# Kernel optimization log

Measured on AMD Instinct MI355X. Metric: run time of the kernel, lower is better.

## Reference

```python
import jax, jax.numpy as jnp
import numpy as np

F = 3          # features
E = 2 * F      # transformer d_model
H = F          # n_heads (head_dim = 2)
FF = 2048      # torch TransformerEncoderLayer default dim_feedforward
OUT = 4
STRIDE = 2
N_BATCH = 16
T_LEN = 2046
LN_EPS = 1e-5


def setup_inputs() -> dict:
    key = jax.random.key(0)
    ks = iter(jax.random.split(key, 48))

    def p(shape, s=0.1):
        return jax.random.normal(next(ks), shape, dtype=jnp.float32) * s

    inp = {
        "x": jax.random.normal(next(ks), (N_BATCH, T_LEN, F), dtype=jnp.float32),
        # multi-scale depthwise conv kernels/biases
        "k64": p((8, F, 64)), "b64": p((8, F)),
        "k16": p((F, 16)), "b16": p((F,)),
        "k8": p((F, 8)), "b8": p((F,)),
        # stage-2 width-3 channel convs
        "kw3": p((F, 3)), "bw3": p((F,)),
        "km3": p((F, 3)), "bm3": p((F,)),
        "kn3": p((F, 3)), "bn3": p((F,)),
        # hidden FCs
        "fc1_w": p((6 * F, 12 * F)), "fc1_b": p((6 * F,)),
        "fc2_w": p((E, 6 * F)), "fc2_b": p((E,)),
        # 2 transformer encoder layers (stacked along leading dim)
        "inw": p((2, 3 * E, E)), "inb": p((2, 3 * E)),
        "ow": p((2, E, E)), "ob": p((2, E)),
        "l1w": jnp.ones((2, E), jnp.float32), "l1b": jnp.zeros((2, E), jnp.float32),
        "l2w": jnp.ones((2, E), jnp.float32), "l2b": jnp.zeros((2, E), jnp.float32),
        "f1w": p((2, FF, E)), "f1b": p((2, FF)),
        "f2w": p((2, E, FF)), "f2b": p((2, E)),
        # output head
        "out1_w": p((7, E)), "out1_b": p((7,)),
        "out2_w": p((OUT, 7)),
    }
    return inp


def _ln(y, w, b):
    mu = y.mean(-1, keepdims=True)
    var = ((y - mu) ** 2).mean(-1, keepdims=True)
    return (y - mu) / jnp.sqrt(var + LN_EPS) * w + b


def _conv3_same(y, k, b):
    # depthwise width-3 'same' conv over seq dim; y:(N,L,F), k:(F,3), b:(F,)
    yp = jnp.pad(y, ((0, 0), (1, 1), (0, 0)))
    return k[:, 0] * yp[:, :-2] + k[:, 1] * yp[:, 1:-1] + k[:, 2] * yp[:, 2:] + b


def _forward(x, k64, b64, k16, b16, k8, b8, kw3, bw3, km3, bm3, kn3, bn3,
             fc1_w, fc1_b, fc2_w, fc2_b, inw, inb, ow, ob,
             l1w, l1b, l2w, l2b, f1w, f1b, f2w, f2b, out1_w, out1_b, out2_w):
    N, T, _ = x.shape
    PAD = 40
    px = jnp.pad(x, ((0, 0), (PAD, PAD), (0, 0)))
    W = T // STRIDE + 1
    centers = PAD + 1 + STRIDE * jnp.arange(W)  # wide window centers
    starts = centers - 32
    relu = jax.nn.relu

    # wide: 8 depthwise width-64 kernels per center -> (N, 8W, F)
    wwin = px[:, centers[:, None] + jnp.arange(-32, 32), :]        # (N,W,64,F)
    wide = jnp.einsum('nwtf,kft->nwkf', wwin, k64) + b64[None, None]
    wide = wide.reshape(N, 8 * W, F)  # center-major, kernel-minor (loop order)

    # mid: width-16 kernel at 8 centers per window -> (N, 8W, F)
    mid_c = (starts[:, None] + 8 * jnp.arange(8)).reshape(-1)
    mwin = px[:, mid_c[:, None] + jnp.arange(-8, 8), :]            # (N,8W,16,F)
    mid = jnp.einsum('nctf,ft->ncf', mwin, k16) + b16

    # narrow: width-8 kernel at 32 centers per window, then maxpool4 -> (N, 8W, F)
    nar_c = (starts[:, None] + 2 * jnp.arange(32)).reshape(-1)
    nwin = px[:, nar_c[:, None] + jnp.arange(-4, 4), :]            # (N,32W,8,F)
    nar = jnp.einsum('nctf,ft->ncf', nwin, k8) + b8
    nar = nar.reshape(N, 8 * W, 4, F).max(axis=2)

    wide = 5.0 * relu(wide)  # residual=0, dropout=0 -> drop is identity
    mid = relu(mid)
    nar = relu(nar)

    wide = relu(_conv3_same(wide, kw3, bw3))
    mid = relu(_conv3_same(mid, km3, bm3))
    nar = relu(_conv3_same(nar, kn3, bn3))

    def pool2(y):  # MaxPool1d(2) over seq dim
        return y.reshape(N, 4 * W, 2, F).max(axis=2)
    wide, mid, nar = pool2(wide), pool2(mid), pool2(nar)

    S = W  # (4W) // 4 blocks

    def blocks(y):  # (N,4W,F) -> (N,S,4F), time-major flatten per block
        return y.reshape(N, S, 4 * F)
    flat = jnp.concatenate([blocks(wide), blocks(mid), blocks(nar)], axis=-1)

    h = relu(flat @ fc1_w.T + fc1_b)  # residual=0 -> (1-residual)*h + 0
    h = relu(h @ fc2_w.T + fc2_b)     # (N,S,E)
    seq = jnp.transpose(h, (1, 0, 2))  # (S,N,E), torch seq-first layout

    d = E // H
    scale = 1.0 / jnp.sqrt(jnp.float32(d))
    for l in range(2):  # post-LN TransformerEncoder, 2 layers
        qkv = seq @ inw[l].T + inb[l]                 # (S,N,3E)
        q, k_, v = jnp.split(qkv, 3, axis=-1)
        q = q.reshape(S, N, H, d)
        k_ = k_.reshape(S, N, H, d)
        v = v.reshape(S, N, H, d)
        att = jnp.einsum('snhd,tnhd->nhst', q, k_) * scale
        p_att = jax.nn.softmax(att, axis=-1)
        o = jnp.einsum('nhst,tnhd->snhd', p_att, v).reshape(S, N, E)
        o = o @ ow[l].T + ob[l]
        seq = _ln(seq + o, l1w[l], l1b[l])
        ff = relu(seq @ f1w[l].T + f1b[l]) @ f2w[l].T + f2b[l]
        seq = _ln(seq + ff, l2w[l], l2b[l])

    pooled = relu(seq.mean(axis=0))           # AvgPool1d over full seq -> (N,E)
    o1 = relu(pooled @ out1_w.T + out1_b)
    logits = o1 @ out2_w.T                    # no bias
    return jax.nn.log_softmax(logits, axis=1)


def reference(x, k64, b64, k16, b16, k8, b8, kw3, bw3, km3, bm3, kn3, bn3,
              fc1_w, fc1_b, fc2_w, fc2_b, inw, inb, ow, ob,
              l1w, l1b, l2w, l2b, f1w, f1b, f2w, f2b, out1_w, out1_b, out2_w):
    return _forward(x, k64, b64, k16, b16, k8, b8, kw3, bw3, km3, bm3, kn3, bn3,
                    fc1_w, fc1_b, fc2_w, fc2_b, inw, inb, ow, ob,
                    l1w, l1b, l2w, l2b, f1w, f1b, f2w, f2b, out1_w, out1_b, out2_w)
```

## Files before the change

kernel.cpp:

```cpp
#include <hip/hip_runtime.h>
#include <math.h>


#define TL 2046
#define SL 1024

__device__ __forceinline__ float relu_(float a){ return fmaxf(a, 0.f); }
__device__ __forceinline__ float fexp2_(float x){ return __builtin_amdgcn_exp2f(x); }
__device__ __forceinline__ float dpp_xadd1(float x){
  return x + __int_as_float(__builtin_amdgcn_update_dpp(
      0, __float_as_int(x), 0xB1, 0xF, 0xF, true));
}
__device__ __forceinline__ float dpp_xadd2(float x){
  return x + __int_as_float(__builtin_amdgcn_update_dpp(
      0, __float_as_int(x), 0x4E, 0xF, 0xF, true));
}

#define SCQK 1.0201265650432017f

__global__ __launch_bounds__(192) void frontend_kernel(
  const float* __restrict__ x, const float* __restrict__ k64,
  const float* __restrict__ b64, const float* __restrict__ k16, const float* __restrict__ b16,
  const float* __restrict__ k8,  const float* __restrict__ b8,
  const float* __restrict__ kw3, const float* __restrict__ bw3,
  const float* __restrict__ km3, const float* __restrict__ bm3,
  const float* __restrict__ kn3, const float* __restrict__ bn3,
  const float* __restrict__ fc1w, const float* __restrict__ fc1b,
  const float* __restrict__ fc2w, const float* __restrict__ fc2b,
  const float* __restrict__ f1w, const float* __restrict__ f1b,
  const float* __restrict__ f2w,
  const float* __restrict__ inw, const float* __restrict__ inb,
  float* __restrict__ fcc, float* __restrict__ seq,
  float4* __restrict__ kv4, float2* __restrict__ qq)
{
  __shared__ float xt[3][200];
  __shared__ float k64s[3*64*8];
  __shared__ float flat_s[64][44];
  __shared__ float h1_s[64][20];
  __shared__ float seq6[64][6];
  const int tid  = threadIdx.x;
  const int f    = tid >> 6;
  const int lane = tid & 63;
  const int n    = blockIdx.x >> 4;
  const int s0   = (blockIdx.x & 15) << 6;
  const int s    = s0 + lane;

  for (int i = blockIdx.x*192 + tid; i < 2*2048*16; i += 256*192){
    int l = i >> 15, r = i & 32767, j = r >> 4, c = r & 15;
    float v = 0.f;
    if (c < 6)       v = f1w[(l*2048 + j)*6 + c];
    else if (c == 6) v = f1b[l*2048 + j];
    else if (c >= 8 && c < 14) v = f2w[(l*6 + (c-8))*2048 + j];
    fcc[i] = v;
  }

  for (int i = tid; i < 600; i += 192){
    int ff = i / 200, pos = i - ff*200;
    int xp = 2*s0 - 39 + pos;
    xt[ff][pos] = (xp >= 0 && xp < TL) ? x[(n*TL + xp)*3 + ff] : 0.f;
  }
  for (int i = tid; i < 1536; i += 192){
    int ff = i >> 9, r = i & 511, t = r >> 3, k = r & 7;
    k64s[i] = k64[k*192 + ff*64 + t];
  }
  __syncthreads();

  float xr[74];
  {
    const int b = 2*lane;
    #pragma unroll
    for (int i = 0; i < 74; i++) xr[i] = xt[f][b + i];
  }

  float accw[8], acc_e0, acc_e1;
  #pragma unroll
  for (int k = 0; k < 8; k++) accw[k] = b64[k*3 + f];
  acc_e0 = accw[7]; acc_e1 = accw[0];
  {
    const float* kp = &k64s[f*512];
    #pragma unroll
    for (int t = 0; t < 64; t++){
      float4 wa = *(const float4*)(kp + t*8);
      float4 wb = *(const float4*)(kp + t*8 + 4);
      float xm = xr[8 + t];
      accw[0] = fmaf(xm, wa.x, accw[0]);
      accw[1] = fmaf(xm, wa.y, accw[1]);
      accw[2] = fmaf(xm, wa.z, accw[2]);
      accw[3] = fmaf(xm, wa.w, accw[3]);
      accw[4] = fmaf(xm, wb.x, accw[4]);
      accw[5] = fmaf(xm, wb.y, accw[5]);
      accw[6] = fmaf(xm, wb.z, accw[6]);
      accw[7] = fmaf(xm, wb.w, accw[7]);
      acc_e0 = fmaf(xr[6 + t],  wb.w, acc_e0);
      acc_e1 = fmaf(xr[10 + t], wa.x, acc_e1);
    }
  }
  float yw[10];
  yw[0] = (s > 0) ? 5.f*relu_(acc_e0) : 0.f;
  #pragma unroll
  for (int c = 1; c <= 8; c++) yw[c] = 5.f*relu_(accw[c-1]);
  yw[9] = (s < 1023) ? 5.f*relu_(acc_e1) : 0.f;

  float w16r[16];
  #pragma unroll
  for (int t = 0; t < 16; t++) w16r[t] = k16[f*16 + t];
  const float bb16 = b16[f];
  float ym[10];
  #pragma unroll
  for (int ci = 0; ci < 10; ci++){
    const int b = (ci == 0) ? 54 : ((ci == 9) ? 2 : 8*(ci-1));
    float a = bb16;
    #pragma unroll
    for (int t = 0; t < 16; t++) a = fmaf(xr[b + t], w16r[t], a);
    ym[ci] = relu_(a);
  }
  if (s == 0)    ym[0] = 0.f;
  if (s == 1023) ym[9] = 0.f;

  float w8r[8];
  #pragma unroll
  for (int t = 0; t < 8; t++) w8r[t] = k8[f*8 + t];
  const float bb8 = b8[f];
  float yn[10];
  #pragma unroll
  for (int ci = 0; ci < 10; ci++){
    float m = -3.0e38f;
    #pragma unroll
    for (int j2 = 0; j2 < 4; j2++){
      const int b = (ci == 0) ? (58 + 2*j2)
                  : ((ci == 9) ? (6 + 2*j2)
                               : (4 + 2*(4*(ci-1) + j2)));
      float a = bb8;
      #pragma unroll
      for (int t = 0; t < 8; t++) a = fmaf(xr[b + t], w8r[t], a);
      m = fmaxf(m, a);
    }
    yn[ci] = relu_(m);
  }
  if (s == 0)    yn[0] = 0.f;
  if (s == 1023) yn[9] = 0.f;

  {
    float c0 = kw3[f*3], c1 = kw3[f*3+1], c2 = kw3[f*3+2], bb = bw3[f];
    #pragma unroll
    for (int q = 0; q < 4; q++){
      float z0 = relu_(fmaf(c0, yw[2*q],   fmaf(c1, yw[2*q+1], fmaf(c2, yw[2*q+2], bb))));
      float z1 = relu_(fmaf(c0, yw[2*q+1], fmaf(c1, yw[2*q+2], fmaf(c2, yw[2*q+3], bb))));
      flat_s[lane][q*3 + f] = fmaxf(z0, z1);
    }
  }
  {
    float c0 = km3[f*3], c1 = km3[f*3+1], c2 = km3[f*3+2], bb = bm3[f];
    #pragma unroll
    for (int q = 0; q < 4; q++){
      float z0 = relu_(fmaf(c0, ym[2*q],   fmaf(c1, ym[2*q+1], fmaf(c2, ym[2*q+2], bb))));
      float z1 = relu_(fmaf(c0, ym[2*q+1], fmaf(c1, ym[2*q+2], fmaf(c2, ym[2*q+3], bb))));
      flat_s[lane][12 + q*3 + f] = fmaxf(z0, z1);
    }
  }
  {
    float c0 = kn3[f*3], c1 = kn3[f*3+1], c2 = kn3[f*3+2], bb = bn3[f];
    #pragma unroll
    for (int q = 0; q < 4; q++){
      float z0 = relu_(fmaf(c0, yn[2*q],   fmaf(c1, yn[2*q+1], fmaf(c2, yn[2*q+2], bb))));
      float z1 = relu_(fmaf(c0, yn[2*q+1], fmaf(c1, yn[2*q+2], fmaf(c2, yn[2*q+3], bb))));
      flat_s[lane][24 + q*3 + f] = fmaxf(z0, z1);
    }
  }
  __syncthreads();

  #pragma unroll
  for (int oi = 0; oi < 6; oi++){
    const int o = 6*f + oi;
    float acc = fc1b[o];
    const float4* wrow = (const float4*)(fc1w + o*36);
    const float4* frow = (const float4*)(&flat_s[lane][0]);
    #pragma unroll
    for (int i = 0; i < 9; i++){
      float4 wv = wrow[i], fv = frow[i];
      acc = fmaf(wv.x, fv.x, acc); acc = fmaf(wv.y, fv.y, acc);
      acc = fmaf(wv.z, fv.z, acc); acc = fmaf(wv.w, fv.w, acc);
    }
    h1_s[lane][o] = relu_(acc);
  }
  __syncthreads();

  #pragma unroll
  for (int ei = 0; ei < 2; ei++){
    const int e = 2*f + ei;
    float acc = fc2b[e];
    #pragma unroll
    for (int o = 0; o < 18; o++) acc = fmaf(h1_s[lane][o], fc2w[e*18 + o], acc);
    float v = acc < 0.f ? 0.f : acc;
    seq[(n*SL + s)*6 + e] = v;
    seq6[lane][e] = v;
  }
  __syncthreads();

  {
    const int g = f;
    float sv[6];
    #pragma unroll
    for (int e = 0; e < 6; e++) sv[e] = seq6[lane][e];
    const int h2 = 2*g;
    float q0 = inb[h2],   q1 = inb[h2+1];
    float k0 = inb[6+h2], k1 = inb[7+h2];
    float v0 = inb[12+h2], v1 = inb[13+h2];
    #pragma unroll
    for (int e = 0; e < 6; e++){
      q0 = fmaf(sv[e], inw[h2*6 + e],      q0);
      q1 = fmaf(sv[e], inw[(h2+1)*6 + e],  q1);
      k0 = fmaf(sv[e], inw[(6+h2)*6 + e],  k0);
      k1 = fmaf(sv[e], inw[(7+h2)*6 + e],  k1);
      v0 = fmaf(sv[e], inw[(12+h2)*6 + e], v0);
      v1 = fmaf(sv[e], inw[(13+h2)*6 + e], v1);
    }
    const int nh = n*3 + g;
    kv4[nh*SL + s] = make_float4(k0*SCQK, k1*SCQK, v0, v1);
    qq [nh*SL + s] = make_float2(q0, q1);
  }
}

__global__ __launch_bounds__(512, 4) void attn_kernel(
  const float4* __restrict__ kv4, const float2* __restrict__ qq,
  float* __restrict__ att_out)
{
  __shared__ float4 sKV[1024];
  __shared__ float red[8][8][8][3];
  const int tid  = threadIdx.x;
  const int w    = tid >> 6;
  const int lane = tid & 63;
  const int rb   = blockIdx.x << 6;
  const int h    = blockIdx.y;
  const int n    = blockIdx.z;
  const int nh   = n*3 + h;

  const float4* kvp = kv4 + nh*SL;
  sKV[tid]       = kvp[tid];
  sKV[tid + 512] = kvp[tid + 512];

  const int r0 = rb + w*8;
  float q0[8], q1[8];
  {
    const float2* qp = qq + nh*SL + r0;
    #pragma unroll
    for (int r = 0; r < 8; r++){ float2 qv = qp[r]; q0[r] = qv.x; q1[r] = qv.y; }
  }
  __syncthreads();

  float lv[8], o0[8], o1[8];
  #pragma unroll
  for (int r = 0; r < 8; r++){ lv[r] = 0.f; o0[r] = 0.f; o1[r] = 0.f; }

  #pragma unroll 2
  for (int i = 0; i < 16; i++){
    float4 K = sKV[i*64 + lane];
    #pragma unroll
    for (int r = 0; r < 8; r++){
      float sc = fmaf(q0[r], K.x, q1[r]*K.y);
      float p  = fexp2_(sc);
      lv[r] += p;
      o0[r] = fmaf(p, K.z, o0[r]);
      o1[r] = fmaf(p, K.w, o1[r]);
    }
  }

  #pragma unroll
  for (int r = 0; r < 8; r++){
    lv[r] = dpp_xadd1(lv[r]); lv[r] = dpp_xadd2(lv[r]); lv[r] += __shfl_xor(lv[r], 4);
    o0[r] = dpp_xadd1(o0[r]); o0[r] = dpp_xadd2(o0[r]); o0[r] += __shfl_xor(o0[r], 4);
    o1[r] = dpp_xadd1(o1[r]); o1[r] = dpp_xadd2(o1[r]); o1[r] += __shfl_xor(o1[r], 4);
  }
  {
    const int g = lane >> 3;
    #pragma unroll
    for (int r = 0; r < 8; r++){
      if ((lane & 7) == r){
        red[w][g][r][0] = lv[r];
        red[w][g][r][1] = o0[r];
        red[w][g][r][2] = o1[r];
      }
    }
  }
  __syncthreads();

  if (tid < 64){
    const int ww = tid >> 3, r = tid & 7;
    float L = 0.f, O0 = 0.f, O1 = 0.f;
    #pragma unroll
    for (int g = 0; g < 8; g++){
      L  += red[ww][g][r][0];
      O0 += red[ww][g][r][1];
      O1 += red[ww][g][r][2];
    }
    const float inv = 1.0f / L;
    float* orow = att_out + (n*SL + rb + tid)*6 + 2*h;
    orow[0] = O0*inv; orow[1] = O1*inv;
  }
}

__global__ __launch_bounds__(512, 4) void ff_kernel(
  const float* __restrict__ seq_in, const float* __restrict__ att,
  const float* __restrict__ fcc,
  const float* __restrict__ ow, const float* __restrict__ ob,
  const float* __restrict__ l1w, const float* __restrict__ l1b,
  float* __restrict__ seq_mid, float* __restrict__ ffp, int layer)
{
  __shared__ float wc[512][16];
  __shared__ float sM[128][6];
  const int tid   = threadIdx.x;
  const int tile  = blockIdx.x >> 2;
  const int slice = blockIdx.x & 3;
  const int tok0  = tile * 128;

  const float4* FC = (const float4*)(fcc + (size_t)(layer*2048 + slice*512)*16);
  for (int i = tid; i < 2048; i += 512)
    ((float4*)wc)[i] = FC[i];

  if (tid < 128){
    const int token = tok0 + tid;
    const float* a  = att + token*6;
    const float* W  = ow + layer*36;
    float av[6];
    #pragma unroll
    for (int e = 0; e < 6; e++) av[e] = a[e];
    float y[6]; float mu = 0.f;
    #pragma unroll
    for (int e = 0; e < 6; e++){
      float o = ob[layer*6 + e];
      #pragma unroll
      for (int e2 = 0; e2 < 6; e2++) o = fmaf(av[e2], W[e*6 + e2], o);
      y[e] = seq_in[token*6 + e] + o;
      mu += y[e];
    }
    mu *= (1.f/6.f);
    float var = 0.f;
    #pragma unroll
    for (int e = 0; e < 6; e++){ float d = y[e] - mu; var = fmaf(d, d, var); }
    var *= (1.f/6.f);
    float rstd = rsqrtf(var + 1e-5f);
    #pragma unroll
    for (int e = 0; e < 6; e++)
      sM[tid][e] = (y[e] - mu)*rstd*l1w[layer*6 + e] + l1b[layer*6 + e];
  }
  __syncthreads();

  const int w = tid >> 6, lane = tid & 63, tp = lane >> 2, ss = lane & 3;

  float sv[8][6];
  {
    const float* sp = &sM[tp*8][0];
    #pragma unroll
    for (int t = 0; t < 8; t++)
      #pragma unroll
      for (int e = 0; e < 6; e++) sv[t][e] = sp[t*6 + e];
  }
  float acc[8][6];
  #pragma unroll
  for (int t = 0; t < 8; t++)
    #pragma unroll
    for (int e = 0; e < 6; e++) acc[t][e] = 0.f;

  const int rbase = w*64 + ss;
  #pragma unroll 2
  for (int i = 0; i < 16; i++){
    const float4* wr = (const float4*)&wc[rbase + i*4][0];
    float4 w0 = wr[0], w1 = wr[1], w2 = wr[2], w3 = wr[3];
    #pragma unroll
    for (int t = 0; t < 8; t++){
      float h = w1.z;
      h = fmaf(sv[t][0], w0.x, h); h = fmaf(sv[t][1], w0.y, h);
      h = fmaf(sv[t][2], w0.z, h); h = fmaf(sv[t][3], w0.w, h);
      h = fmaf(sv[t][4], w1.x, h); h = fmaf(sv[t][5], w1.y, h);
      h = relu_(h);
      acc[t][0] = fmaf(h, w2.x, acc[t][0]); acc[t][1] = fmaf(h, w2.y, acc[t][1]);
      acc[t][2] = fmaf(h, w2.z, acc[t][2]); acc[t][3] = fmaf(h, w2.w, acc[t][3]);
      acc[t][4] = fmaf(h, w3.x, acc[t][4]); acc[t][5] = fmaf(h, w3.y, acc[t][5]);
    }
  }

  #pragma unroll
  for (int t = 0; t < 8; t++)
    #pragma unroll
    for (int e = 0; e < 6; e++){
      acc[t][e] = dpp_xadd1(acc[t][e]);
      acc[t][e] = dpp_xadd2(acc[t][e]);
    }
  __syncthreads();
  float* red = (float*)wc;
  if (ss == 0){
    #pragma unroll
    for (int t = 0; t < 8; t++)
      #pragma unroll
      for (int e = 0; e < 6; e++) red[(w*16 + tp)*48 + t*6 + e] = acc[t][e];
  }
  __syncthreads();
  for (int i = tid; i < 768; i += 512){
    const int tl = i / 6, e = i - tl*6;
    const int rtp = tl >> 3, rt = tl & 7;
    float sum = 0.f;
    #pragma unroll
    for (int wv = 0; wv < 8; wv++)
      sum += red[(wv*16 + rtp)*48 + rt*6 + e];
    ffp[(size_t)(slice*16384 + tok0 + tl)*6 + e] = sum;
  }
  if (slice == 0 && tid < 128){
    #pragma unroll
    for (int e = 0; e < 6; e++) seq_mid[(tok0 + tid)*6 + e] = sM[tid][e];
  }
}

__global__ __launch_bounds__(128) void ffln_kernel(
  const float* __restrict__ seq_mid, const float* __restrict__ ffp,
  const float* __restrict__ f2b, const float* __restrict__ lw,
  const float* __restrict__ lb,
  const float* __restrict__ Wq, const float* __restrict__ Bq,
  float* __restrict__ seq_out, float4* __restrict__ kv4, float2* __restrict__ qq)
{
  const int tok = blockIdx.x*128 + threadIdx.x;
  float y[6]; float mu = 0.f;
  #pragma unroll
  for (int e = 0; e < 6; e++){
    float v = seq_mid[tok*6 + e] + f2b[e];
    v += ffp[(size_t)(0*16384 + tok)*6 + e];
    v += ffp[(size_t)(1*16384 + tok)*6 + e];
    v += ffp[(size_t)(2*16384 + tok)*6 + e];
    v += ffp[(size_t)(3*16384 + tok)*6 + e];
    y[e] = v; mu += v;
  }
  mu *= (1.f/6.f);
  float var = 0.f;
  #pragma unroll
  for (int e = 0; e < 6; e++){ float d = y[e] - mu; var = fmaf(d, d, var); }
  var *= (1.f/6.f);
  float rstd = rsqrtf(var + 1e-5f);
  float sv[6];
  #pragma unroll
  for (int e = 0; e < 6; e++){
    sv[e] = (y[e] - mu)*rstd*lw[e] + lb[e];
    seq_out[tok*6 + e] = sv[e];
  }

  const int n = tok >> 10, t = tok & 1023;
  #pragma unroll
  for (int g = 0; g < 3; g++){
    const int h2 = 2*g;
    float q0 = Bq[h2],   q1 = Bq[h2+1];
    float k0 = Bq[6+h2], k1 = Bq[7+h2];
    float v0 = Bq[12+h2], v1 = Bq[13+h2];
    #pragma unroll
    for (int e = 0; e < 6; e++){
      q0 = fmaf(sv[e], Wq[h2*6 + e],      q0);
      q1 = fmaf(sv[e], Wq[(h2+1)*6 + e],  q1);
      k0 = fmaf(sv[e], Wq[(6+h2)*6 + e],  k0);
      k1 = fmaf(sv[e], Wq[(7+h2)*6 + e],  k1);
      v0 = fmaf(sv[e], Wq[(12+h2)*6 + e], v0);
      v1 = fmaf(sv[e], Wq[(13+h2)*6 + e], v1);
    }
    const int nh = n*3 + g;
    kv4[nh*SL + t] = make_float4(k0*SCQK, k1*SCQK, v0, v1);
    qq [nh*SL + t] = make_float2(q0, q1);
  }
}

__global__ __launch_bounds__(256) void final_kernel(
  const float* __restrict__ seq_mid, const float* __restrict__ ffp,
  const float* __restrict__ f2b, const float* __restrict__ lw,
  const float* __restrict__ lb,
  const float* __restrict__ o1w, const float* __restrict__ o1b,
  const float* __restrict__ o2w, float* __restrict__ out)
{
  __shared__ float fred[4][6];
  __shared__ float pooled[6];
  const int n = blockIdx.x, tid = threadIdx.x;
  float psum[6] = {0,0,0,0,0,0};

  #pragma unroll
  for (int i = 0; i < 4; i++){
    const int tok = n*SL + tid + i*256;
    float y[6]; float mu = 0.f;
    #pragma unroll
    for (int e = 0; e < 6; e++){
      float v = seq_mid[tok*6 + e] + f2b[e];
      v += ffp[(size_t)(0*16384 + tok)*6 + e];
      v += ffp[(size_t)(1*16384 + tok)*6 + e];
      v += ffp[(size_t)(2*16384 + tok)*6 + e];
      v += ffp[(size_t)(3*16384 + tok)*6 + e];
      y[e] = v; mu += v;
    }
    mu *= (1.f/6.f);
    float var = 0.f;
    #pragma unroll
    for (int e = 0; e < 6; e++){ float d = y[e] - mu; var = fmaf(d, d, var); }
    var *= (1.f/6.f);
    float rstd = rsqrtf(var + 1e-5f);
    #pragma unroll
    for (int e = 0; e < 6; e++)
      psum[e] += (y[e] - mu)*rstd*lw[e] + lb[e];
  }

  #pragma unroll
  for (int e = 0; e < 6; e++){
    psum[e] += __shfl_xor(psum[e], 1);  psum[e] += __shfl_xor(psum[e], 2);
    psum[e] += __shfl_xor(psum[e], 4);  psum[e] += __shfl_xor(psum[e], 8);
    psum[e] += __shfl_xor(psum[e], 16); psum[e] += __shfl_xor(psum[e], 32);
  }
  if ((tid & 63) == 0){
    #pragma unroll
    for (int e = 0; e < 6; e++) fred[tid >> 6][e] = psum[e];
  }
  __syncthreads();
  if (tid < 6){
    float t = fred[0][tid] + fred[1][tid] + fred[2][tid] + fred[3][tid];
    pooled[tid] = fmaxf(t * (1.f/1024.f), 0.f);
  }
  __syncthreads();
  if (tid == 0){
    float o1[7];
    #pragma unroll
    for (int o = 0; o < 7; o++){
      float a = o1b[o];
      #pragma unroll
      for (int e2 = 0; e2 < 6; e2++) a = fmaf(pooled[e2], o1w[o*6 + e2], a);
      o1[o] = relu_(a);
    }
    float lg[4];
    #pragma unroll
    for (int c = 0; c < 4; c++){
      float a = 0.f;
      #pragma unroll
      for (int o = 0; o < 7; o++) a = fmaf(o1[o], o2w[c*7 + o], a);
      lg[c] = a;
    }
    float m = fmaxf(fmaxf(lg[0], lg[1]), fmaxf(lg[2], lg[3]));
    float sum = 0.f;
    #pragma unroll
    for (int c = 0; c < 4; c++) sum += expf(lg[c] - m);
    float lse = m + logf(sum);
    #pragma unroll
    for (int c = 0; c < 4; c++) out[n*4 + c] = lg[c] - lse;
  }
}

extern "C" void kernel_launch(void* const* d_in, const int* in_sizes, int n_in,
                              void* d_out, int out_size, void* d_ws, size_t ws_size,
                              hipStream_t stream)
{
  const float* x    = (const float*)d_in[0];
  const float* k64  = (const float*)d_in[1];
  const float* b64  = (const float*)d_in[2];
  const float* k16  = (const float*)d_in[3];
  const float* b16  = (const float*)d_in[4];
  const float* k8   = (const float*)d_in[5];
  const float* b8   = (const float*)d_in[6];
  const float* kw3  = (const float*)d_in[7];
  const float* bw3  = (const float*)d_in[8];
  const float* km3  = (const float*)d_in[9];
  const float* bm3  = (const float*)d_in[10];
  const float* kn3  = (const float*)d_in[11];
  const float* bn3  = (const float*)d_in[12];
  const float* fc1w = (const float*)d_in[13];
  const float* fc1b = (const float*)d_in[14];
  const float* fc2w = (const float*)d_in[15];
  const float* fc2b = (const float*)d_in[16];
  const float* inw  = (const float*)d_in[17];
  const float* inb  = (const float*)d_in[18];
  const float* ow   = (const float*)d_in[19];
  const float* ob   = (const float*)d_in[20];
  const float* l1w  = (const float*)d_in[21];
  const float* l1b  = (const float*)d_in[22];
  const float* l2w  = (const float*)d_in[23];
  const float* l2b  = (const float*)d_in[24];
  const float* f1w  = (const float*)d_in[25];
  const float* f1b  = (const float*)d_in[26];
  const float* f2w  = (const float*)d_in[27];
  const float* f2b  = (const float*)d_in[28];
  const float* o1w  = (const float*)d_in[29];
  const float* o1b  = (const float*)d_in[30];
  const float* o2w  = (const float*)d_in[31];
  float* out = (float*)d_out;

  float* w = (float*)d_ws;
  float*  seq_a   = w;
  float*  seq_b   = w + 98304;
  float*  att     = w + 196608;
  float*  seq_mid = w + 294912;
  float*  ffp     = w + 393216;
  float*  fcc     = w + 786432;
  float4* kv4     = (float4*)(w + 851968);
  float2* qq      = (float2*)(w + 1048576);

  frontend_kernel<<<256, 192, 0, stream>>>(x, k64, b64, k16, b16, k8, b8,
      kw3, bw3, km3, bm3, kn3, bn3, fc1w, fc1b, fc2w, fc2b,
      f1w, f1b, f2w, inw, inb, fcc, seq_a, kv4, qq);

  dim3 agrid(16, 3, 16);
  attn_kernel<<<agrid, 512, 0, stream>>>(kv4, qq, att);
  ff_kernel<<<512, 512, 0, stream>>>(seq_a, att, fcc, ow, ob, l1w, l1b,
      seq_mid, ffp, 0);
  ffln_kernel<<<128, 128, 0, stream>>>(seq_mid, ffp, f2b, l2w, l2b,
      inw + 108, inb + 18, seq_b, kv4, qq);

  attn_kernel<<<agrid, 512, 0, stream>>>(kv4, qq, att);
  ff_kernel<<<512, 512, 0, stream>>>(seq_b, att, fcc, ow, ob, l1w, l1b,
      seq_mid, ffp, 1);
  final_kernel<<<16, 256, 0, stream>>>(seq_mid, ffp, f2b + 6, l2w + 6, l2b + 6,
      o1w, o1b, o2w, out);
}
```

Baseline: 77.67 us.

## Split frontend conv work across wave halves and double frontend grid

The frontend kernel now handles 32 output positions per block instead of 64. The two halves of each wave split the taps of the 64-wide, 16-wide and 8-wide convolutions, combine partial sums (or maxes) with a cross-lane shuffle, and divide the FC and QKV outputs between them. The grid grows to 512 blocks to use more CUs and shorten the per-thread serial chain, at the cost of extra shuffles and duplicated xr loads. The unroll factor of the attention and FF inner loops is also raised from 2 to 4.

Result: slower. 96.00 us (+23.6%).

```diff
diff --git a/kernel.cpp b/kernel.cpp
--- a/kernel.cpp
+++ b/kernel.cpp
@@ -33,19 +33,21 @@
   float* __restrict__ fcc, float* __restrict__ seq,
   float4* __restrict__ kv4, float2* __restrict__ qq)
 {
-  __shared__ float xt[3][200];
+  __shared__ float xt[3][136];
   __shared__ float k64s[3*64*8];
-  __shared__ float flat_s[64][44];
-  __shared__ float h1_s[64][20];
-  __shared__ float seq6[64][6];
+  __shared__ float flat_s[32][44];
+  __shared__ float h1_s[32][20];
+  __shared__ float seq6[32][6];
   const int tid  = threadIdx.x;
   const int f    = tid >> 6;
   const int lane = tid & 63;
-  const int n    = blockIdx.x >> 4;
-  const int s0   = (blockIdx.x & 15) << 6;
-  const int s    = s0 + lane;
-
-  for (int i = blockIdx.x*192 + tid; i < 2*2048*16; i += 256*192){
+  const int tk   = lane & 31;
+  const int hh   = lane >> 5;
+  const int n    = blockIdx.x >> 5;
+  const int s0   = (blockIdx.x & 31) << 5;
+  const int s    = s0 + tk;
+
+  for (int i = blockIdx.x*192 + tid; i < 2*2048*16; i += 512*192){
     int l = i >> 15, r = i & 32767, j = r >> 4, c = r & 15;
     float v = 0.f;
     if (c < 6)       v = f1w[(l*2048 + j)*6 + c];
@@ -54,8 +56,8 @@
     fcc[i] = v;
   }
 
-  for (int i = tid; i < 600; i += 192){
-    int ff = i / 200, pos = i - ff*200;
+  for (int i = tid; i < 408; i += 192){
+    int ff = i / 136, pos = i - ff*136;
     int xp = 2*s0 - 39 + pos;
     xt[ff][pos] = (xp >= 0 && xp < TL) ? x[(n*TL + xp)*3 + ff] : 0.f;
   }
@@ -67,19 +69,19 @@
 
   float xr[74];
   {
-    const int b = 2*lane;
+    const int b = 2*tk;
     #pragma unroll
     for (int i = 0; i < 74; i++) xr[i] = xt[f][b + i];
   }
 
-  float accw[8], acc_e0, acc_e1;
-  #pragma unroll
-  for (int k = 0; k < 8; k++) accw[k] = b64[k*3 + f];
-  acc_e0 = accw[7]; acc_e1 = accw[0];
+  float accw[8] = {0,0,0,0,0,0,0,0};
+  float acc_e0 = 0.f, acc_e1 = 0.f;
   {
     const float* kp = &k64s[f*512];
-    #pragma unroll
-    for (int t = 0; t < 64; t++){
+    const int t0 = hh*32;
+    #pragma unroll
+    for (int ti = 0; ti < 32; ti++){
+      const int t = t0 + ti;
       float4 wa = *(const float4*)(kp + t*8);
       float4 wb = *(const float4*)(kp + t*8 + 4);
       float xm = xr[8 + t];
@@ -95,24 +97,33 @@
       acc_e1 = fmaf(xr[10 + t], wa.x, acc_e1);
     }
   }
+  #pragma unroll
+  for (int k = 0; k < 8; k++){
+    accw[k] += __shfl_xor(accw[k], 32);
+    accw[k] += b64[k*3 + f];
+  }
+  acc_e0 += __shfl_xor(acc_e0, 32);  acc_e0 += b64[7*3 + f];
+  acc_e1 += __shfl_xor(acc_e1, 32);  acc_e1 += b64[f];
+
   float yw[10];
   yw[0] = (s > 0) ? 5.f*relu_(acc_e0) : 0.f;
   #pragma unroll
   for (int c = 1; c <= 8; c++) yw[c] = 5.f*relu_(accw[c-1]);
   yw[9] = (s < 1023) ? 5.f*relu_(acc_e1) : 0.f;
 
-  float w16r[16];
-  #pragma unroll
-  for (int t = 0; t < 16; t++) w16r[t] = k16[f*16 + t];
+  float w16r[8];
+  #pragma unroll
+  for (int t = 0; t < 8; t++) w16r[t] = k16[f*16 + hh*8 + t];
   const float bb16 = b16[f];
   float ym[10];
   #pragma unroll
   for (int ci = 0; ci < 10; ci++){
-    const int b = (ci == 0) ? 54 : ((ci == 9) ? 2 : 8*(ci-1));
-    float a = bb16;
-    #pragma unroll
-    for (int t = 0; t < 16; t++) a = fmaf(xr[b + t], w16r[t], a);
-    ym[ci] = relu_(a);
+    const int b = ((ci == 0) ? 54 : ((ci == 9) ? 2 : 8*(ci-1))) + hh*8;
+    float a = 0.f;
+    #pragma unroll
+    for (int t = 0; t < 8; t++) a = fmaf(xr[b + t], w16r[t], a);
+    a += __shfl_xor(a, 32);
+    ym[ci] = relu_(a + bb16);
   }
   if (s == 0)    ym[0] = 0.f;
   if (s == 1023) ym[9] = 0.f;
@@ -126,7 +137,8 @@
   for (int ci = 0; ci < 10; ci++){
     float m = -3.0e38f;
     #pragma unroll
-    for (int j2 = 0; j2 < 4; j2++){
+    for (int jj = 0; jj < 2; jj++){
+      const int j2 = hh*2 + jj;
       const int b = (ci == 0) ? (58 + 2*j2)
                   : ((ci == 9) ? (6 + 2*j2)
                                : (4 + 2*(4*(ci-1) + j2)));
@@ -135,65 +147,62 @@
       for (int t = 0; t < 8; t++) a = fmaf(xr[b + t], w8r[t], a);
       m = fmaxf(m, a);
     }
+    m = fmaxf(m, __shfl_xor(m, 32));
     yn[ci] = relu_(m);
   }
   if (s == 0)    yn[0] = 0.f;
   if (s == 1023) yn[9] = 0.f;
 
-  {
+  if (hh == 0){
     float c0 = kw3[f*3], c1 = kw3[f*3+1], c2 = kw3[f*3+2], bb = bw3[f];
     #pragma unroll
     for (int q = 0; q < 4; q++){
       float z0 = relu_(fmaf(c0, yw[2*q],   fmaf(c1, yw[2*q+1], fmaf(c2, yw[2*q+2], bb))));
       float z1 = relu_(fmaf(c0, yw[2*q+1], fmaf(c1, yw[2*q+2], fmaf(c2, yw[2*q+3], bb))));
-      flat_s[lane][q*3 + f] = fmaxf(z0, z1);
-    }
-  }
-  {
-    float c0 = km3[f*3], c1 = km3[f*3+1], c2 = km3[f*3+2], bb = bm3[f];
+      flat_s[tk][q*3 + f] = fmaxf(z0, z1);
+    }
+    float d0 = km3[f*3], d1 = km3[f*3+1], d2 = km3[f*3+2], db = bm3[f];
     #pragma unroll
     for (int q = 0; q < 4; q++){
-      float z0 = relu_(fmaf(c0, ym[2*q],   fmaf(c1, ym[2*q+1], fmaf(c2, ym[2*q+2], bb))));
-      float z1 = relu_(fmaf(c0, ym[2*q+1], fmaf(c1, ym[2*q+2], fmaf(c2, ym[2*q+3], bb))));
-      flat_s[lane][12 + q*3 + f] = fmaxf(z0, z1);
-    }
-  }
-  {
+      float z0 = relu_(fmaf(d0, ym[2*q],   fmaf(d1, ym[2*q+1], fmaf(d2, ym[2*q+2], db))));
+      float z1 = relu_(fmaf(d0, ym[2*q+1], fmaf(d1, ym[2*q+2], fmaf(d2, ym[2*q+3], db))));
+      flat_s[tk][12 + q*3 + f] = fmaxf(z0, z1);
+    }
+  } else {
     float c0 = kn3[f*3], c1 = kn3[f*3+1], c2 = kn3[f*3+2], bb = bn3[f];
     #pragma unroll
     for (int q = 0; q < 4; q++){
       float z0 = relu_(fmaf(c0, yn[2*q],   fmaf(c1, yn[2*q+1], fmaf(c2, yn[2*q+2], bb))));
       float z1 = relu_(fmaf(c0, yn[2*q+1], fmaf(c1, yn[2*q+2], fmaf(c2, yn[2*q+3], bb))));
-      flat_s[lane][24 + q*3 + f] = fmaxf(z0, z1);
-    }
-  }
-  __syncthreads();
-
-  #pragma unroll
-  for (int oi = 0; oi < 6; oi++){
-    const int o = 6*f + oi;
+      flat_s[tk][24 + q*3 + f] = fmaxf(z0, z1);
+    }
+  }
+  __syncthreads();
+
+  #pragma unroll
+  for (int oi = 0; oi < 3; oi++){
+    const int o = 6*f + 3*hh + oi;
     float acc = fc1b[o];
     const float4* wrow = (const float4*)(fc1w + o*36);
-    const float4* frow = (const float4*)(&flat_s[lane][0]);
+    const float4* frow = (const float4*)(&flat_s[tk][0]);
     #pragma unroll
     for (int i = 0; i < 9; i++){
       float4 wv = wrow[i], fv = frow[i];
       acc = fmaf(wv.x, fv.x, acc); acc = fmaf(wv.y, fv.y, acc);
       acc = fmaf(wv.z, fv.z, acc); acc = fmaf(wv.w, fv.w, acc);
     }
-    h1_s[lane][o] = relu_(acc);
-  }
-  __syncthreads();
-
-  #pragma unroll
-  for (int ei = 0; ei < 2; ei++){
-    const int e = 2*f + ei;
+    h1_s[tk][o] = relu_(acc);
+  }
+  __syncthreads();
+
+  {
+    const int e = 2*f + hh;
     float acc = fc2b[e];
     #pragma unroll
-    for (int o = 0; o < 18; o++) acc = fmaf(h1_s[lane][o], fc2w[e*18 + o], acc);
+    for (int o = 0; o < 18; o++) acc = fmaf(h1_s[tk][o], fc2w[e*18 + o], acc);
     float v = acc < 0.f ? 0.f : acc;
     seq[(n*SL + s)*6 + e] = v;
-    seq6[lane][e] = v;
+    seq6[tk][e] = v;
   }
   __syncthreads();
 
@@ -201,23 +210,20 @@
     const int g = f;
     float sv[6];
     #pragma unroll
-    for (int e = 0; e < 6; e++) sv[e] = seq6[lane][e];
+    for (int e = 0; e < 6; e++) sv[e] = seq6[tk][e];
     const int h2 = 2*g;
-    float q0 = inb[h2],   q1 = inb[h2+1];
-    float k0 = inb[6+h2], k1 = inb[7+h2];
-    float v0 = inb[12+h2], v1 = inb[13+h2];
+    const int rq = h2 + hh, rk = 6 + h2 + hh, rv = 12 + h2 + hh;
+    float qv = inb[rq], kv = inb[rk], vv = inb[rv];
     #pragma unroll
     for (int e = 0; e < 6; e++){
-      q0 = fmaf(sv[e], inw[h2*6 + e],      q0);
-      q1 = fmaf(sv[e], inw[(h2+1)*6 + e],  q1);
-      k0 = fmaf(sv[e], inw[(6+h2)*6 + e],  k0);
-      k1 = fmaf(sv[e], inw[(7+h2)*6 + e],  k1);
-      v0 = fmaf(sv[e], inw[(12+h2)*6 + e], v0);
-      v1 = fmaf(sv[e], inw[(13+h2)*6 + e], v1);
-    }
-    const int nh = n*3 + g;
-    kv4[nh*SL + s] = make_float4(k0*SCQK, k1*SCQK, v0, v1);
-    qq [nh*SL + s] = make_float2(q0, q1);
+      qv = fmaf(sv[e], inw[rq*6 + e], qv);
+      kv = fmaf(sv[e], inw[rk*6 + e], kv);
+      vv = fmaf(sv[e], inw[rv*6 + e], vv);
+    }
+    const int idx = (n*3 + g)*SL + s;
+    ((float*)qq)[idx*2 + hh]       = qv;
+    ((float*)kv4)[idx*4 + hh]      = kv*SCQK;
+    ((float*)kv4)[idx*4 + 2 + hh]  = vv;
   }
 }
 
@@ -252,7 +258,7 @@
   #pragma unroll
   for (int r = 0; r < 8; r++){ lv[r] = 0.f; o0[r] = 0.f; o1[r] = 0.f; }
 
-  #pragma unroll 2
+  #pragma unroll 4
   for (int i = 0; i < 16; i++){
     float4 K = sKV[i*64 + lane];
     #pragma unroll
@@ -362,7 +368,7 @@
     for (int e = 0; e < 6; e++) acc[t][e] = 0.f;
 
   const int rbase = w*64 + ss;
-  #pragma unroll 2
+  #pragma unroll 4
   for (int i = 0; i < 16; i++){
     const float4* wr = (const float4*)&wc[rbase + i*4][0];
     float4 w0 = wr[0], w1 = wr[1], w2 = wr[2], w3 = wr[3];
@@ -590,7 +596,7 @@
   float4* kv4     = (float4*)(w + 851968);
   float2* qq      = (float2*)(w + 1048576);
 
-  frontend_kernel<<<256, 192, 0, stream>>>(x, k64, b64, k16, b16, k8, b8,
+  frontend_kernel<<<512, 192, 0, stream>>>(x, k64, b64, k16, b16, k8, b8,
       kw3, bw3, km3, bm3, kn3, bn3, fc1w, fc1b, fc2w, fc2b,
       f1w, f1b, f2w, inw, inb, fcc, seq_a, kv4, qq);
 
```
